# Kernel tuning notes

Measured on AMD Instinct MI355X. Metric: run time of the kernel, lower is better.

## Reference

```python
import jax, jax.numpy as jnp
import numpy as np

N, E = 20000, 640000
IN_CH, OUT_CH = 128, 64
HEADS = (4, 4)
NEG_SLOPE = 0.2


def _gat_layer(x, src, dst, edge_attr, edge_atten, W, a_src, a_dst, W_e, a_e, b, H, C, n_nodes):
    # x: [N, F_in] -> per-head features [N, H, C]
    xh = (x @ W).reshape(-1, H, C)
    alpha_src = jnp.sum(xh * a_src, axis=-1)          # [N, H]
    alpha_dst = jnp.sum(xh * a_dst, axis=-1)          # [N, H]
    eemb = (edge_attr @ W_e).reshape(-1, H, C)        # [E, H, C]
    alpha_e = jnp.sum(eemb * a_e, axis=-1)            # [E, H]
    alpha = alpha_src[src] + alpha_dst[dst] + alpha_e # [E, H]
    alpha = jax.nn.leaky_relu(alpha, NEG_SLOPE)
    # softmax over variable-degree neighborhoods (segments keyed by dst)
    amax = jax.ops.segment_max(alpha, dst, num_segments=n_nodes)
    alpha = jnp.exp(alpha - amax[dst])
    denom = jax.ops.segment_sum(alpha, dst, num_segments=n_nodes)
    alpha = alpha / (denom[dst] + 1e-16)
    msg = xh[src] * alpha[:, :, None]                 # [E, H, C]
    msg = msg * edge_atten[:, :, None]                # edge_atten: [E, 1] -> broadcast over H, C
    out = jax.ops.segment_sum(msg, dst, num_segments=n_nodes)
    out = out.reshape(n_nodes, H * C) + b
    return out, alpha


def setup_inputs() -> dict:
    key = jax.random.key(0)
    ks = jax.random.split(key, 16)
    H1, H2 = HEADS
    d1_in, d1_out = IN_CH, H1 * OUT_CH
    d2_in, d2_out = H1 * OUT_CH, H2 * OUT_CH
    s = lambda fi: 1.0 / np.sqrt(fi)
    inp = {
        "x": jax.random.normal(ks[0], (N, IN_CH), jnp.float32),
        "edge_index": jax.random.randint(ks[1], (2, E), 0, N, jnp.int64 if jax.config.jax_enable_x64 else jnp.int32),
        "batch": jnp.zeros((N,), jnp.int32),
        "edge_attr": jax.random.normal(ks[2], (E, 1), jnp.float32),
        "edge_atten": jax.random.uniform(ks[3], (E, 1), jnp.float32),
        # layer 1 params
        "W1": jax.random.normal(ks[4], (d1_in, d1_out), jnp.float32) * s(d1_in),
        "a_src1": jax.random.normal(ks[5], (H1, OUT_CH), jnp.float32) * s(OUT_CH),
        "a_dst1": jax.random.normal(ks[6], (H1, OUT_CH), jnp.float32) * s(OUT_CH),
        "W_e1": jax.random.normal(ks[7], (1, d1_out), jnp.float32),
        "a_e1": jax.random.normal(ks[8], (H1, OUT_CH), jnp.float32) * s(OUT_CH),
        "b1": jnp.zeros((d1_out,), jnp.float32),
        # layer 2 params
        "W2": jax.random.normal(ks[9], (d2_in, d2_out), jnp.float32) * s(d2_in),
        "a_src2": jax.random.normal(ks[10], (H2, OUT_CH), jnp.float32) * s(OUT_CH),
        "a_dst2": jax.random.normal(ks[11], (H2, OUT_CH), jnp.float32) * s(OUT_CH),
        "W_e2": jax.random.normal(ks[12], (1, d2_out), jnp.float32),
        "a_e2": jax.random.normal(ks[13], (H2, OUT_CH), jnp.float32) * s(OUT_CH),
        "b2": jnp.zeros((d2_out,), jnp.float32),
    }
    return inp


def reference(x, edge_index, batch, edge_attr, edge_atten,
              W1, a_src1, a_dst1, W_e1, a_e1, b1,
              W2, a_src2, a_dst2, W_e2, a_e2, b2):
    src, dst = edge_index[0], edge_index[1]
    h, w1 = _gat_layer(x, src, dst, edge_attr, edge_atten,
                       W1, a_src1, a_dst1, W_e1, a_e1, b1, HEADS[0], OUT_CH, N)
    h, w2 = _gat_layer(h, src, dst, edge_attr, edge_atten,
                       W2, a_src2, a_dst2, W_e2, a_e2, b2, HEADS[1], OUT_CH, N)
    return h, w1, w2
```

## Files before the change

### kernel.cpp

```cpp
#include <hip/hip_runtime.h>
#include <math.h>

#define NEG_SLOPE 0.2f
#define CAP 128
#define ST  136
#define NNODES 20000
#define NB 128

typedef short s16x8 __attribute__((ext_vector_type(8)));
typedef unsigned short us8 __attribute__((ext_vector_type(8)));
typedef float f32x4 __attribute__((ext_vector_type(4)));

__device__ __forceinline__ unsigned short f2bf(float f) {
    unsigned int u = __float_as_uint(f);
    return (unsigned short)((u + 0x7FFFu + ((u >> 16) & 1u)) >> 16);
}
__device__ __forceinline__ float bf2f(unsigned short s) {
    return __uint_as_float(((unsigned int)s) << 16);
}

__global__ __launch_bounds__(512) void hist_prep(const int* __restrict__ dst,
                                                 int* __restrict__ ghist,
                                                 int E, int chunk, int N, int histB,
                                                 const float* __restrict__ x,
                                                 const float* __restrict__ W1,
                                                 const float* __restrict__ W2,
                                                 const float* __restrict__ W_e1,
                                                 const float* __restrict__ a_e1,
                                                 const float* __restrict__ W_e2,
                                                 const float* __restrict__ a_e2,
                                                 unsigned short* __restrict__ xb16,
                                                 unsigned short* __restrict__ Wt1,
                                                 unsigned short* __restrict__ Wt2,
                                                 float* __restrict__ ce) {
    __shared__ int h[NNODES / 2];
    if ((int)blockIdx.x < histB) {
        const int b = blockIdx.x;
        const int NH = N >> 1;
        for (int i = threadIdx.x; i < NH; i += 512) h[i] = 0;
        __syncthreads();
        const int e0 = b * chunk;
        const int e1 = min(e0 + chunk, E);
        for (int e = e0 + (int)threadIdx.x; e < e1; e += 512) {
            int d = dst[e];
            atomicAdd(&h[d >> 1], 1 << ((d & 1) << 4));
        }
        __syncthreads();
        int2* out = (int2*)(ghist + (size_t)b * N);
        for (int i = threadIdx.x; i < NH; i += 512) {
            int v = h[i];
            out[i] = make_int2(v & 0xFFFF, ((unsigned)v) >> 16);
        }
    } else {
        const int p = (int)blockIdx.x - histB;
        const int gsz = 256 * 512;
        const int gid = p * 512 + (int)threadIdx.x;
        for (int i = gid; i < 128 * 256; i += gsz) {
            int k = i >> 8, n = i & 255;
            Wt1[n * 128 + k] = f2bf(W1[i]);
        }
        for (int i = gid; i < 256 * 256; i += gsz) {
            int k = i >> 8, n = i & 255;
            Wt2[n * 256 + k] = f2bf(W2[i]);
        }
        for (int i = gid; i < N * 32; i += gsz) {
            float4 f = ((const float4*)x)[i];
            ushort4 u = make_ushort4(f2bf(f.x), f2bf(f.y), f2bf(f.z), f2bf(f.w));
            ((ushort4*)xb16)[i] = u;
        }
        if (p < 2 && threadIdx.x < 256) {
            const float* We = p == 0 ? W_e1 : W_e2;
            const float* ae = p == 0 ? a_e1 : a_e2;
            int hh = threadIdx.x >> 6, c = threadIdx.x & 63;
            float pr = We[hh * 64 + c] * ae[hh * 64 + c];
#pragma unroll
            for (int off = 32; off > 0; off >>= 1) pr += __shfl_down(pr, off);
            if (c == 0) ce[p * 4 + hh] = pr;
        }
    }
}

__device__ __forceinline__ void gemm_core(const unsigned short* __restrict__ A16,
                                          const unsigned short* __restrict__ Bt16,
                                          unsigned short* __restrict__ C16,
                                          const float* __restrict__ a_src,
                                          const float* __restrict__ a_dst,
                                          float* __restrict__ asrc,
                                          float* __restrict__ adst,
                                          int M, int K, int bx, int by,
                                          unsigned short (*As)[40],
                                          unsigned short (*Bs)[40]) {
    const int tid = threadIdx.x;
    const int w = tid >> 6, l = tid & 63;
    const int quad = l >> 4, m16 = l & 15;
    const int row0 = by * 128, col0 = bx * 64;

    f32x4 acc[2][4] = {};

    const int a_r = tid >> 1;
    const int a_k = (tid & 1) * 16;
    const int b_n = tid >> 2;
    const int b_k = (tid & 3) * 8;

    for (int k0 = 0; k0 < K; k0 += 32) {
        int gr = row0 + a_r; if (gr > M - 1) gr = M - 1;
        const unsigned short* ap = A16 + (size_t)gr * K + k0 + a_k;
        *(us8*)&As[a_r][a_k]     = *(const us8*)ap;
        *(us8*)&As[a_r][a_k + 8] = *(const us8*)(ap + 8);
        *(us8*)&Bs[b_n][b_k] = *(const us8*)(Bt16 + (size_t)(col0 + b_n) * K + k0 + b_k);
        __syncthreads();

        s16x8 af[2], bfr[4];
#pragma unroll
        for (int mt = 0; mt < 2; ++mt)
            af[mt] = *(const s16x8*)&As[w * 32 + mt * 16 + m16][quad * 8];
#pragma unroll
        for (int nt = 0; nt < 4; ++nt)
            bfr[nt] = *(const s16x8*)&Bs[nt * 16 + m16][quad * 8];
#pragma unroll
        for (int mt = 0; mt < 2; ++mt)
#pragma unroll
            for (int nt = 0; nt < 4; ++nt)
                acc[mt][nt] = __builtin_amdgcn_mfma_f32_16x16x32_bf16(af[mt], bfr[nt], acc[mt][nt], 0, 0, 0);
        __syncthreads();
    }

    const int h = bx;
    float was[4], wad[4];
#pragma unroll
    for (int nt = 0; nt < 4; ++nt) {
        int c = nt * 16 + m16;
        was[nt] = a_src[h * 64 + c];
        wad[nt] = a_dst[h * 64 + c];
    }

#pragma unroll
    for (int mt = 0; mt < 2; ++mt)
#pragma unroll
        for (int i = 0; i < 4; ++i) {
            int row = row0 + w * 32 + mt * 16 + quad * 4 + i;
            float ps = 0.f, pd = 0.f;
#pragma unroll
            for (int nt = 0; nt < 4; ++nt) {
                float v = acc[mt][nt][i];
                ps += v * was[nt];
                pd += v * wad[nt];
            }
#pragma unroll
            for (int ofs = 1; ofs < 16; ofs <<= 1) {
                ps += __shfl_xor(ps, ofs);
                pd += __shfl_xor(pd, ofs);
            }
            if (m16 == 0 && row < M) {
                asrc[(size_t)row * 4 + h] = ps;
                adst[(size_t)row * 4 + h] = pd;
            }
        }

#pragma unroll
    for (int mt = 0; mt < 2; ++mt)
#pragma unroll
        for (int nt = 0; nt < 4; ++nt) {
            int col = col0 + nt * 16 + m16;
#pragma unroll
            for (int i = 0; i < 4; ++i) {
                int row = row0 + w * 32 + mt * 16 + quad * 4 + i;
                if (row < M) C16[(size_t)row * 256 + col] = f2bf(acc[mt][nt][i]);
            }
        }
}

__global__ __launch_bounds__(256) void gemm1_scan(const unsigned short* __restrict__ A16,
                                                  const unsigned short* __restrict__ Bt16,
                                                  unsigned short* __restrict__ C16,
                                                  const float* __restrict__ a_src,
                                                  const float* __restrict__ a_dst,
                                                  float* __restrict__ asrc,
                                                  float* __restrict__ adst,
                                                  int M, int K, int gemmB,
                                                  int* __restrict__ ghist,
                                                  int* __restrict__ deg,
                                                  int N, int histB) {
    __shared__ unsigned short As[128][40];
    __shared__ unsigned short Bs[64][40];
    if ((int)blockIdx.x < gemmB) {
        gemm_core(A16, Bt16, C16, a_src, a_dst, asrc, adst, M, K,
                  blockIdx.x & 3, blockIdx.x >> 2, As, Bs);
    } else {
        int bin = ((int)blockIdx.x - gemmB) * 256 + (int)threadIdx.x;
        if (bin < N) {
            int run = 0;
            for (int b = 0; b < histB; b += 8) {
                int v[8];
#pragma unroll
                for (int j = 0; j < 8; ++j) v[j] = ghist[(b + j) * N + bin];
#pragma unroll
                for (int j = 0; j < 8; ++j) { ghist[(b + j) * N + bin] = run; run += v[j]; }
            }
            deg[bin] = run;
        }
    }
}

__global__ __launch_bounds__(1024) void fill_scan(const int* __restrict__ src,
                                                  const int* __restrict__ dst,
                                                  const float* __restrict__ edge_attr,
                                                  const float* __restrict__ edge_atten,
                                                  const int* __restrict__ deg,
                                                  const int* __restrict__ ghist,
                                                  int* __restrict__ off_out,
                                                  int4* __restrict__ rec,
                                                  int E, int chunk, int N) {
    __shared__ int base[NNODES];
    __shared__ int wsum[16];
    __shared__ int woff[16];
    __shared__ int s_carry, s_bt;
    if (threadIdx.x == 0) s_carry = 0;
    __syncthreads();
    const int lane = threadIdx.x & 63, wid = threadIdx.x >> 6;
    for (int bb = 0; bb < N; bb += 4096) {
        int i0 = bb + (int)threadIdx.x * 4;
        int v0 = (i0 + 0 < N) ? deg[i0 + 0] : 0;
        int v1 = (i0 + 1 < N) ? deg[i0 + 1] : 0;
        int v2 = (i0 + 2 < N) ? deg[i0 + 2] : 0;
        int v3 = (i0 + 3 < N) ? deg[i0 + 3] : 0;
        int tsum = v0 + v1 + v2 + v3;
        int incl = tsum;
#pragma unroll
        for (int ofs = 1; ofs < 64; ofs <<= 1) {
            int t = __shfl_up(incl, ofs);
            if (lane >= ofs) incl += t;
        }
        if (lane == 63) wsum[wid] = incl;
        __syncthreads();
        if (wid == 0) {
            int ws = (lane < 16) ? wsum[lane] : 0;
            int wincl = ws;
#pragma unroll
            for (int ofs = 1; ofs < 16; ofs <<= 1) {
                int t = __shfl_up(wincl, ofs);
                if (lane >= ofs) wincl += t;
            }
            if (lane < 16) woff[lane] = wincl - ws;
            if (lane == 15) s_bt = wincl;
        }
        __syncthreads();
        int e0 = s_carry + woff[wid] + incl - tsum;
        int e1 = e0 + v0, e2 = e1 + v1, e3 = e2 + v2;
        if (i0 + 0 < N) base[i0 + 0] = e0;
        if (i0 + 1 < N) base[i0 + 1] = e1;
        if (i0 + 2 < N) base[i0 + 2] = e2;
        if (i0 + 3 < N) base[i0 + 3] = e3;
        __syncthreads();
        if (threadIdx.x == 0) s_carry += s_bt;
        __syncthreads();
    }
    if (blockIdx.x == 0) {
        for (int i = threadIdx.x; i < N; i += 1024) off_out[i] = base[i];
        if (threadIdx.x == 0) off_out[N] = s_carry;
    }
    const int b = blockIdx.x;
    const int* part = ghist + (size_t)b * N;
    for (int i = threadIdx.x; i < N; i += 1024) base[i] += part[i];
    __syncthreads();
    const int e0c = b * chunk;
    const int e1c = min(e0c + chunk, E);
    for (int e = e0c + (int)threadIdx.x; e < e1c; e += 1024) {
        int d = dst[e];
        int pos = atomicAdd(&base[d], 1);
        rec[pos] = make_int4(src[e], e, __float_as_int(edge_attr[e]),
                             __float_as_int(edge_atten[e]));
    }
}

__global__ __launch_bounds__(256) void node_fused(const int4* __restrict__ rec,
                                                  const int* __restrict__ off,
                                                  const float* __restrict__ asrc,
                                                  const float* __restrict__ adst,
                                                  const float* __restrict__ ce,
                                                  const unsigned short* __restrict__ xh16,
                                                  const float* __restrict__ bias,
                                                  float* __restrict__ w,
                                                  int write_w,
                                                  float* __restrict__ mxrc,
                                                  float* __restrict__ houtf,
                                                  unsigned short* __restrict__ hout16,
                                                  int N) {
    __shared__ float s_al[4][4][ST];
    __shared__ int s_src[4][CAP];
    const int wid = threadIdx.x >> 6;
    const int n = blockIdx.x * 4 + wid;
    if (n >= N) return;
    const int lane = threadIdx.x & 63;
    float* al = &s_al[wid][0][0];
    int* sv = s_src[wid];
    const int o0 = off[n], o1 = off[n + 1];
    const int deg = o1 - o0;

    const float4 c4 = *(const float4*)ce;
    const float4 ad4 = *(const float4*)(adst + (size_t)n * 4);

    if (deg <= 64) {
        int4 r; float4 a;
        a.x = a.y = a.z = a.w = -3.4e38f;
        if (lane < deg) {
            r = rec[o0 + lane];
            float ea = __int_as_float(r.z);
            const float4 as4 = *(const float4*)(asrc + (size_t)r.x * 4);
            a.x = as4.x + ad4.x + ea * c4.x;
            a.y = as4.y + ad4.y + ea * c4.y;
            a.z = as4.z + ad4.z + ea * c4.z;
            a.w = as4.w + ad4.w + ea * c4.w;
            a.x = a.x > 0.f ? a.x : NEG_SLOPE * a.x;
            a.y = a.y > 0.f ? a.y : NEG_SLOPE * a.y;
            a.z = a.z > 0.f ? a.z : NEG_SLOPE * a.z;
            a.w = a.w > 0.f ? a.w : NEG_SLOPE * a.w;
        }
        float4 mx = a;
#pragma unroll
        for (int ofs = 1; ofs < 64; ofs <<= 1) {
            mx.x = fmaxf(mx.x, __shfl_xor(mx.x, ofs));
            mx.y = fmaxf(mx.y, __shfl_xor(mx.y, ofs));
            mx.z = fmaxf(mx.z, __shfl_xor(mx.z, ofs));
            mx.w = fmaxf(mx.w, __shfl_xor(mx.w, ofs));
        }
        float4 ex = make_float4(0.f, 0.f, 0.f, 0.f);
        if (lane < deg) {
            ex.x = __expf(a.x - mx.x);
            ex.y = __expf(a.y - mx.y);
            ex.z = __expf(a.z - mx.z);
            ex.w = __expf(a.w - mx.w);
        }
        float4 sm = ex;
#pragma unroll
        for (int ofs = 1; ofs < 64; ofs <<= 1) {
            sm.x += __shfl_xor(sm.x, ofs);
            sm.y += __shfl_xor(sm.y, ofs);
            sm.z += __shfl_xor(sm.z, ofs);
            sm.w += __shfl_xor(sm.w, ofs);
        }
        float4 rc;
        rc.x = 1.f / (sm.x + 1e-16f);
        rc.y = 1.f / (sm.y + 1e-16f);
        rc.z = 1.f / (sm.z + 1e-16f);
        rc.w = 1.f / (sm.w + 1e-16f);
        if (mxrc && lane == 0) {
            *(float4*)(mxrc + (size_t)n * 8) = mx;
            *(float4*)(mxrc + (size_t)n * 8 + 4) = rc;
        }
        if (lane < deg) {
            float4 aln;
            aln.x = ex.x * rc.x;
            aln.y = ex.y * rc.y;
            aln.z = ex.z * rc.z;
            aln.w = ex.w * rc.w;
            if (write_w) *(float4*)(w + (size_t)r.y * 4) = aln;
            float att = __int_as_float(r.w);
            sv[lane] = r.x;
            al[0 * ST + lane] = aln.x * att;
            al[1 * ST + lane] = aln.y * att;
            al[2 * ST + lane] = aln.z * att;
            al[3 * ST + lane] = aln.w * att;
        }
    } else {
        float4 mx = make_float4(-3.4e38f, -3.4e38f, -3.4e38f, -3.4e38f);
        for (int idx = lane; idx < deg; idx += 64) {
            int4 r = rec[o0 + idx];
            float ea = __int_as_float(r.z);
            const float4 as4 = *(const float4*)(asrc + (size_t)r.x * 4);
            float4 a;
            a.x = as4.x + ad4.x + ea * c4.x;
            a.y = as4.y + ad4.y + ea * c4.y;
            a.z = as4.z + ad4.z + ea * c4.z;
            a.w = as4.w + ad4.w + ea * c4.w;
            a.x = a.x > 0.f ? a.x : NEG_SLOPE * a.x;
            a.y = a.y > 0.f ? a.y : NEG_SLOPE * a.y;
            a.z = a.z > 0.f ? a.z : NEG_SLOPE * a.z;
            a.w = a.w > 0.f ? a.w : NEG_SLOPE * a.w;
            if (idx < CAP) {
                sv[idx] = r.x;
                al[0 * ST + idx] = a.x;
                al[1 * ST + idx] = a.y;
                al[2 * ST + idx] = a.z;
                al[3 * ST + idx] = a.w;
            } else {
                *(float4*)(w + (size_t)r.y * 4) = a;
            }
            mx.x = fmaxf(mx.x, a.x);
            mx.y = fmaxf(mx.y, a.y);
            mx.z = fmaxf(mx.z, a.z);
            mx.w = fmaxf(mx.w, a.w);
        }
#pragma unroll
        for (int ofs = 1; ofs < 64; ofs <<= 1) {
            mx.x = fmaxf(mx.x, __shfl_xor(mx.x, ofs));
            mx.y = fmaxf(mx.y, __shfl_xor(mx.y, ofs));
            mx.z = fmaxf(mx.z, __shfl_xor(mx.z, ofs));
            mx.w = fmaxf(mx.w, __shfl_xor(mx.w, ofs));
        }
        float4 sm = make_float4(0.f, 0.f, 0.f, 0.f);
        for (int idx = lane; idx < deg; idx += 64) {
            float4 a;
            int espill = -1;
            if (idx < CAP) {
                a.x = al[0 * ST + idx];
                a.y = al[1 * ST + idx];
                a.z = al[2 * ST + idx];
                a.w = al[3 * ST + idx];
            } else {
                espill = rec[o0 + idx].y;
                a = *(const float4*)(w + (size_t)espill * 4);
            }
            a.x = __expf(a.x - mx.x);
            a.y = __expf(a.y - mx.y);
            a.z = __expf(a.z - mx.z);
            a.w = __expf(a.w - mx.w);
            if (idx < CAP) {
                al[0 * ST + idx] = a.x;
                al[1 * ST + idx] = a.y;
                al[2 * ST + idx] = a.z;
                al[3 * ST + idx] = a.w;
            } else {
                *(float4*)(w + (size_t)espill * 4) = a;
            }
            sm.x += a.x; sm.y += a.y; sm.z += a.z; sm.w += a.w;
        }
#pragma unroll
        for (int ofs = 1; ofs < 64; ofs <<= 1) {
            sm.x += __shfl_xor(sm.x, ofs);
            sm.y += __shfl_xor(sm.y, ofs);
            sm.z += __shfl_xor(sm.z, ofs);
            sm.w += __shfl_xor(sm.w, ofs);
        }
        float4 rc;
        rc.x = 1.f / (sm.x + 1e-16f);
        rc.y = 1.f / (sm.y + 1e-16f);
        rc.z = 1.f / (sm.z + 1e-16f);
        rc.w = 1.f / (sm.w + 1e-16f);
        if (mxrc && lane == 0) {
            *(float4*)(mxrc + (size_t)n * 8) = mx;
            *(float4*)(mxrc + (size_t)n * 8 + 4) = rc;
        }
        for (int idx = lane; idx < deg; idx += 64) {
            int4 r = rec[o0 + idx];
            float4 ex;
            if (idx < CAP) {
                ex.x = al[0 * ST + idx];
                ex.y = al[1 * ST + idx];
                ex.z = al[2 * ST + idx];
                ex.w = al[3 * ST + idx];
            } else {
                ex = *(const float4*)(w + (size_t)r.y * 4);
            }
            float4 aln;
            aln.x = ex.x * rc.x;
            aln.y = ex.y * rc.y;
            aln.z = ex.z * rc.z;
            aln.w = ex.w * rc.w;
            *(float4*)(w + (size_t)r.y * 4) = aln;
            if (idx < CAP) {
                float att = __int_as_float(r.w);
                al[0 * ST + idx] = aln.x * att;
                al[1 * ST + idx] = aln.y * att;
                al[2 * ST + idx] = aln.z * att;
                al[3 * ST + idx] = aln.w * att;
            }
        }
    }

    const int hh = lane >> 4;
    const float* alh = al + hh * ST;
    float4 a0 = *(const float4*)(bias + lane * 4);
    float4 a1 = make_float4(0.f, 0.f, 0.f, 0.f);
    float4 a2 = a1, a3 = a1;
    const int kmax = deg < CAP ? deg : CAP;
    int k = 0;
    for (; k + 8 <= kmax; k += 8) {
        int4 s4a = *(const int4*)&sv[k];
        int4 s4b = *(const int4*)&sv[k + 4];
        float4 ca = *(const float4*)&alh[k];
        float4 cb = *(const float4*)&alh[k + 4];
        ushort4 u0 = *((const ushort4*)(xh16 + (size_t)s4a.x * 256) + lane);
        ushort4 u1 = *((const ushort4*)(xh16 + (size_t)s4a.y * 256) + lane);
        ushort4 u2 = *((const ushort4*)(xh16 + (size_t)s4a.z * 256) + lane);
        ushort4 u3 = *((const ushort4*)(xh16 + (size_t)s4a.w * 256) + lane);
        ushort4 u4 = *((const ushort4*)(xh16 + (size_t)s4b.x * 256) + lane);
        ushort4 u5 = *((const ushort4*)(xh16 + (size_t)s4b.y * 256) + lane);
        ushort4 u6 = *((const ushort4*)(xh16 + (size_t)s4b.z * 256) + lane);
        ushort4 u7 = *((const ushort4*)(xh16 + (size_t)s4b.w * 256) + lane);
        a0.x += bf2f(u0.x) * ca.x; a0.y += bf2f(u0.y) * ca.x; a0.z += bf2f(u0.z) * ca.x; a0.w += bf2f(u0.w) * ca.x;
        a1.x += bf2f(u1.x) * ca.y; a1.y += bf2f(u1.y) * ca.y; a1.z += bf2f(u1.z) * ca.y; a1.w += bf2f(u1.w) * ca.y;
        a2.x += bf2f(u2.x) * ca.z; a2.y += bf2f(u2.y) * ca.z; a2.z += bf2f(u2.z) * ca.z; a2.w += bf2f(u2.w) * ca.z;
        a3.x += bf2f(u3.x) * ca.w; a3.y += bf2f(u3.y) * ca.w; a3.z += bf2f(u3.z) * ca.w; a3.w += bf2f(u3.w) * ca.w;
        a0.x += bf2f(u4.x) * cb.x; a0.y += bf2f(u4.y) * cb.x; a0.z += bf2f(u4.z) * cb.x; a0.w += bf2f(u4.w) * cb.x;
        a1.x += bf2f(u5.x) * cb.y; a1.y += bf2f(u5.y) * cb.y; a1.z += bf2f(u5.z) * cb.y; a1.w += bf2f(u5.w) * cb.y;
        a2.x += bf2f(u6.x) * cb.z; a2.y += bf2f(u6.y) * cb.z; a2.z += bf2f(u6.z) * cb.z; a2.w += bf2f(u6.w) * cb.z;
        a3.x += bf2f(u7.x) * cb.w; a3.y += bf2f(u7.y) * cb.w; a3.z += bf2f(u7.z) * cb.w; a3.w += bf2f(u7.w) * cb.w;
    }
    for (; k + 4 <= kmax; k += 4) {
        int4 s4 = *(const int4*)&sv[k];
        float4 cc = *(const float4*)&alh[k];
        ushort4 u0 = *((const ushort4*)(xh16 + (size_t)s4.x * 256) + lane);
        ushort4 u1 = *((const ushort4*)(xh16 + (size_t)s4.y * 256) + lane);
        ushort4 u2 = *((const ushort4*)(xh16 + (size_t)s4.z * 256) + lane);
        ushort4 u3 = *((const ushort4*)(xh16 + (size_t)s4.w * 256) + lane);
        a0.x += bf2f(u0.x) * cc.x; a0.y += bf2f(u0.y) * cc.x; a0.z += bf2f(u0.z) * cc.x; a0.w += bf2f(u0.w) * cc.x;
        a1.x += bf2f(u1.x) * cc.y; a1.y += bf2f(u1.y) * cc.y; a1.z += bf2f(u1.z) * cc.y; a1.w += bf2f(u1.w) * cc.y;
        a2.x += bf2f(u2.x) * cc.z; a2.y += bf2f(u2.y) * cc.z; a2.z += bf2f(u2.z) * cc.z; a2.w += bf2f(u2.w) * cc.z;
        a3.x += bf2f(u3.x) * cc.w; a3.y += bf2f(u3.y) * cc.w; a3.z += bf2f(u3.z) * cc.w; a3.w += bf2f(u3.w) * cc.w;
    }
    for (; k < kmax; ++k) {
        int s = sv[k];
        float sc = alh[k];
        ushort4 uv = *((const ushort4*)(xh16 + (size_t)s * 256) + lane);
        a0.x += bf2f(uv.x) * sc; a0.y += bf2f(uv.y) * sc;
        a0.z += bf2f(uv.z) * sc; a0.w += bf2f(uv.w) * sc;
    }
    for (k = CAP; k < deg; ++k) {
        int4 r = rec[o0 + k];
        float sc = w[(size_t)r.y * 4 + hh] * __int_as_float(r.w);
        ushort4 uv = *((const ushort4*)(xh16 + (size_t)r.x * 256) + lane);
        a0.x += bf2f(uv.x) * sc; a0.y += bf2f(uv.y) * sc;
        a0.z += bf2f(uv.z) * sc; a0.w += bf2f(uv.w) * sc;
    }
    float4 acc;
    acc.x = (a0.x + a1.x) + (a2.x + a3.x);
    acc.y = (a0.y + a1.y) + (a2.y + a3.y);
    acc.z = (a0.z + a1.z) + (a2.z + a3.z);
    acc.w = (a0.w + a1.w) + (a2.w + a3.w);
    if (houtf)  *(float4*)(houtf + (size_t)n * 256 + lane * 4) = acc;
    if (hout16) {
        ushort4 u = make_ushort4(f2bf(acc.x), f2bf(acc.y), f2bf(acc.z), f2bf(acc.w));
        *((ushort4*)(hout16 + (size_t)n * 256) + lane) = u;
    }
}

__global__ __launch_bounds__(256) void gemm2_w1(const unsigned short* __restrict__ A16,
                                                const unsigned short* __restrict__ Bt16,
                                                unsigned short* __restrict__ C16,
                                                const float* __restrict__ a_src,
                                                const float* __restrict__ a_dst,
                                                float* __restrict__ asrc2,
                                                float* __restrict__ adst2,
                                                int M, int K, int gemmB,
                                                const int* __restrict__ src,
                                                const int* __restrict__ dstp,
                                                const float* __restrict__ edge_attr,
                                                const float* __restrict__ asrc1,
                                                const float* __restrict__ adst1,
                                                const float* __restrict__ mxrc,
                                                const float* __restrict__ ce1,
                                                float* __restrict__ w1, int E) {
    __shared__ unsigned short As[128][40];
    __shared__ unsigned short Bs[64][40];
    if ((int)blockIdx.x < gemmB) {
        gemm_core(A16, Bt16, C16, a_src, a_dst, asrc2, adst2, M, K,
                  blockIdx.x & 3, blockIdx.x >> 2, As, Bs);
    } else {
        const int stride = ((int)gridDim.x - gemmB) * 256;
        const float4 c4 = *(const float4*)ce1;
        for (int e = ((int)blockIdx.x - gemmB) * 256 + (int)threadIdx.x; e < E; e += stride) {
            int s = src[e], d = dstp[e];
            float ea = edge_attr[e];
            const float4 as4 = *(const float4*)(asrc1 + (size_t)s * 4);
            const float4 ad4 = *(const float4*)(adst1 + (size_t)d * 4);
            float4 a;
            a.x = as4.x + ad4.x + ea * c4.x;
            a.y = as4.y + ad4.y + ea * c4.y;
            a.z = as4.z + ad4.z + ea * c4.z;
            a.w = as4.w + ad4.w + ea * c4.w;
            a.x = a.x > 0.f ? a.x : NEG_SLOPE * a.x;
            a.y = a.y > 0.f ? a.y : NEG_SLOPE * a.y;
            a.z = a.z > 0.f ? a.z : NEG_SLOPE * a.z;
            a.w = a.w > 0.f ? a.w : NEG_SLOPE * a.w;
            const float4 mx = *(const float4*)(mxrc + (size_t)d * 8);
            const float4 rc = *(const float4*)(mxrc + (size_t)d * 8 + 4);
            float4 o;
            o.x = __expf(a.x - mx.x) * rc.x;
            o.y = __expf(a.y - mx.y) * rc.y;
            o.z = __expf(a.z - mx.z) * rc.z;
            o.w = __expf(a.w - mx.w) * rc.w;
            *(float4*)(w1 + (size_t)e * 4) = o;
        }
    }
}

extern "C" void kernel_launch(void* const* d_in, const int* in_sizes, int n_in,
                              void* d_out, int out_size, void* d_ws, size_t ws_size,
                              hipStream_t stream) {
    const float* x          = (const float*)d_in[0];
    const int*   ei         = (const int*)d_in[1];
    const float* edge_attr  = (const float*)d_in[3];
    const float* edge_atten = (const float*)d_in[4];
    const float* W1     = (const float*)d_in[5];
    const float* a_src1 = (const float*)d_in[6];
    const float* a_dst1 = (const float*)d_in[7];
    const float* W_e1   = (const float*)d_in[8];
    const float* a_e1   = (const float*)d_in[9];
    const float* b1     = (const float*)d_in[10];
    const float* W2     = (const float*)d_in[11];
    const float* a_src2 = (const float*)d_in[12];
    const float* a_dst2 = (const float*)d_in[13];
    const float* W_e2   = (const float*)d_in[14];
    const float* a_e2   = (const float*)d_in[15];
    const float* b2     = (const float*)d_in[16];

    const int N = in_sizes[0] / 128;
    const int E = in_sizes[1] / 2;
    const int* srcp = ei;
    const int* dstp = ei + E;

    char* ws = (char*)d_ws;
    int4* rec             = (int4*)ws;            ws += (size_t)E * 16;
    unsigned short* xh16  = (unsigned short*)ws;  ws += (size_t)N * 256 * 2;
    unsigned short* h116  = (unsigned short*)ws;  ws += (size_t)N * 256 * 2;
    unsigned short* Wt1   = (unsigned short*)ws;  ws += (size_t)256 * 128 * 2;
    unsigned short* Wt2   = (unsigned short*)ws;  ws += (size_t)256 * 256 * 2;
    float* asrc   = (float*)ws;                   ws += (size_t)N * 4 * 4;
    float* adst   = (float*)ws;                   ws += (size_t)N * 4 * 4;
    float* asrc2  = (float*)ws;                   ws += (size_t)N * 4 * 4;
    float* adst2  = (float*)ws;                   ws += (size_t)N * 4 * 4;
    float* mxrc   = (float*)ws;                   ws += (size_t)N * 8 * 4;
    float* ce     = (float*)ws;                   ws += 32;
    int* deg    = (int*)ws;                       ws += (size_t)N * 4;
    int* off    = (int*)ws;                       ws += (size_t)(N + 1) * 4;
    int* ghist  = (int*)ws;                       ws += (size_t)NB * N * 4;

    unsigned short* xb16 = h116;

    float* hout2 = (float*)d_out;
    float* w1    = hout2 + (size_t)N * 256;
    float* w2    = w1 + (size_t)E * 4;

    const int chunk = (E + NB - 1) / NB;
    const int gb = (N + 3) / 4;
    const int rows = (N + 127) / 128;
    const int gemmB = 4 * rows;
    const int scanB = (N + 255) / 256;
    const int wB = 512;

    hist_prep<<<NB + 256, 512, 0, stream>>>(dstp, ghist, E, chunk, N, NB,
                                            x, W1, W2, W_e1, a_e1, W_e2, a_e2,
                                            xb16, Wt1, Wt2, ce);
    gemm1_scan<<<gemmB + scanB, 256, 0, stream>>>(xb16, Wt1, xh16, a_src1, a_dst1,
                                                  asrc, adst, N, 128, gemmB,
                                                  ghist, deg, N, NB);
    fill_scan<<<NB, 1024, 0, stream>>>(srcp, dstp, edge_attr, edge_atten,
                                       deg, ghist, off, rec, E, chunk, N);
    node_fused<<<gb, 256, 0, stream>>>(rec, off, asrc, adst, ce, xh16, b1, w1,
                                       0, mxrc, (float*)nullptr, h116, N);
    gemm2_w1<<<gemmB + wB, 256, 0, stream>>>(h116, Wt2, xh16, a_src2, a_dst2,
                                             asrc2, adst2, N, 256, gemmB,
                                             srcp, dstp, edge_attr,
                                             asrc, adst, mxrc, ce, w1, E);
    node_fused<<<gb, 256, 0, stream>>>(rec, off, asrc2, adst2, ce + 4, xh16, b2, w2,
                                       1, (float*)nullptr, hout2,
                                       (unsigned short*)nullptr, N);
}
```

Baseline: 253.6 us.

## Widen GEMM tiles to 128x128 with K-step 64 and halve histogram blocks

The shared GEMM core now computes a 128x128 output tile per block, covering two heads, with a K step of 64. Each block therefore does more MFMA work per shared-memory load and per barrier, and the grid has half as many GEMM blocks. The per-head attention projections are split inside each tile. Separately, the number of histogram chunks drops from 128 to 64, which shrinks the per-bin scan and the ghist buffer but leaves fewer blocks for the histogram and fill stages. The cost is more registers (16 accumulators) and more LDS per block, which may lower occupancy.

After: 263.3 us. +3.8%, slower.

```diff
diff --git a/kernel.cpp b/kernel.cpp
--- a/kernel.cpp
+++ b/kernel.cpp
@@ -5,7 +5,7 @@
 #define CAP 128
 #define ST  136
 #define NNODES 20000
-#define NB 128
+#define NB 64
 
 typedef short s16x8 __attribute__((ext_vector_type(8)));
 typedef unsigned short us8 __attribute__((ext_vector_type(8)));
@@ -88,48 +88,56 @@
                                           float* __restrict__ asrc,
                                           float* __restrict__ adst,
                                           int M, int K, int bx, int by,
-                                          unsigned short (*As)[40],
-                                          unsigned short (*Bs)[40]) {
+                                          unsigned short (*As)[72],
+                                          unsigned short (*Bs)[72]) {
     const int tid = threadIdx.x;
     const int w = tid >> 6, l = tid & 63;
     const int quad = l >> 4, m16 = l & 15;
-    const int row0 = by * 128, col0 = bx * 64;
-
-    f32x4 acc[2][4] = {};
+    const int row0 = by * 128, col0 = bx * 128;
+
+    f32x4 acc[2][8] = {};
 
     const int a_r = tid >> 1;
-    const int a_k = (tid & 1) * 16;
-    const int b_n = tid >> 2;
-    const int b_k = (tid & 3) * 8;
-
-    for (int k0 = 0; k0 < K; k0 += 32) {
+    const int a_k = (tid & 1) * 32;
+
+    for (int k0 = 0; k0 < K; k0 += 64) {
         int gr = row0 + a_r; if (gr > M - 1) gr = M - 1;
         const unsigned short* ap = A16 + (size_t)gr * K + k0 + a_k;
-        *(us8*)&As[a_r][a_k]     = *(const us8*)ap;
-        *(us8*)&As[a_r][a_k + 8] = *(const us8*)(ap + 8);
-        *(us8*)&Bs[b_n][b_k] = *(const us8*)(Bt16 + (size_t)(col0 + b_n) * K + k0 + b_k);
-        __syncthreads();
-
-        s16x8 af[2], bfr[4];
-#pragma unroll
-        for (int mt = 0; mt < 2; ++mt)
-            af[mt] = *(const s16x8*)&As[w * 32 + mt * 16 + m16][quad * 8];
-#pragma unroll
-        for (int nt = 0; nt < 4; ++nt)
-            bfr[nt] = *(const s16x8*)&Bs[nt * 16 + m16][quad * 8];
-#pragma unroll
-        for (int mt = 0; mt < 2; ++mt)
-#pragma unroll
-            for (int nt = 0; nt < 4; ++nt)
-                acc[mt][nt] = __builtin_amdgcn_mfma_f32_16x16x32_bf16(af[mt], bfr[nt], acc[mt][nt], 0, 0, 0);
-        __syncthreads();
-    }
-
-    const int h = bx;
-    float was[4], wad[4];
-#pragma unroll
-    for (int nt = 0; nt < 4; ++nt) {
-        int c = nt * 16 + m16;
+        *(us8*)&As[a_r][a_k]      = *(const us8*)ap;
+        *(us8*)&As[a_r][a_k + 8]  = *(const us8*)(ap + 8);
+        *(us8*)&As[a_r][a_k + 16] = *(const us8*)(ap + 16);
+        *(us8*)&As[a_r][a_k + 24] = *(const us8*)(ap + 24);
+        const unsigned short* bp = Bt16 + (size_t)(col0 + a_r) * K + k0 + a_k;
+        *(us8*)&Bs[a_r][a_k]      = *(const us8*)bp;
+        *(us8*)&Bs[a_r][a_k + 8]  = *(const us8*)(bp + 8);
+        *(us8*)&Bs[a_r][a_k + 16] = *(const us8*)(bp + 16);
+        *(us8*)&Bs[a_r][a_k + 24] = *(const us8*)(bp + 24);
+        __syncthreads();
+
+#pragma unroll
+        for (int sub = 0; sub < 2; ++sub) {
+            s16x8 af[2], bfr[8];
+#pragma unroll
+            for (int mt = 0; mt < 2; ++mt)
+                af[mt] = *(const s16x8*)&As[w * 32 + mt * 16 + m16][sub * 32 + quad * 8];
+#pragma unroll
+            for (int nt = 0; nt < 8; ++nt)
+                bfr[nt] = *(const s16x8*)&Bs[nt * 16 + m16][sub * 32 + quad * 8];
+#pragma unroll
+            for (int mt = 0; mt < 2; ++mt)
+#pragma unroll
+                for (int nt = 0; nt < 8; ++nt)
+                    acc[mt][nt] = __builtin_amdgcn_mfma_f32_16x16x32_bf16(af[mt], bfr[nt], acc[mt][nt], 0, 0, 0);
+        }
+        __syncthreads();
+    }
+
+    const int h0 = col0 >> 6;
+    float was[8], wad[8];
+#pragma unroll
+    for (int nt = 0; nt < 8; ++nt) {
+        int h = h0 + (nt >> 2);
+        int c = (nt & 3) * 16 + m16;
         was[nt] = a_src[h * 64 + c];
         wad[nt] = a_dst[h * 64 + c];
     }
@@ -139,28 +147,31 @@
 #pragma unroll
         for (int i = 0; i < 4; ++i) {
             int row = row0 + w * 32 + mt * 16 + quad * 4 + i;
-            float ps = 0.f, pd = 0.f;
-#pragma unroll
-            for (int nt = 0; nt < 4; ++nt) {
-                float v = acc[mt][nt][i];
-                ps += v * was[nt];
-                pd += v * wad[nt];
-            }
-#pragma unroll
-            for (int ofs = 1; ofs < 16; ofs <<= 1) {
-                ps += __shfl_xor(ps, ofs);
-                pd += __shfl_xor(pd, ofs);
-            }
-            if (m16 == 0 && row < M) {
-                asrc[(size_t)row * 4 + h] = ps;
-                adst[(size_t)row * 4 + h] = pd;
+#pragma unroll
+            for (int p = 0; p < 2; ++p) {
+                float ps = 0.f, pd = 0.f;
+#pragma unroll
+                for (int nt = p * 4; nt < p * 4 + 4; ++nt) {
+                    float v = acc[mt][nt][i];
+                    ps += v * was[nt];
+                    pd += v * wad[nt];
+                }
+#pragma unroll
+                for (int ofs = 1; ofs < 16; ofs <<= 1) {
+                    ps += __shfl_xor(ps, ofs);
+                    pd += __shfl_xor(pd, ofs);
+                }
+                if (m16 == 0 && row < M) {
+                    asrc[(size_t)row * 4 + h0 + p] = ps;
+                    adst[(size_t)row * 4 + h0 + p] = pd;
+                }
             }
         }
 
 #pragma unroll
     for (int mt = 0; mt < 2; ++mt)
 #pragma unroll
-        for (int nt = 0; nt < 4; ++nt) {
+        for (int nt = 0; nt < 8; ++nt) {
             int col = col0 + nt * 16 + m16;
 #pragma unroll
             for (int i = 0; i < 4; ++i) {
@@ -181,11 +192,11 @@
                                                   int* __restrict__ ghist,
                                                   int* __restrict__ deg,
                                                   int N, int histB) {
-    __shared__ unsigned short As[128][40];
-    __shared__ unsigned short Bs[64][40];
+    __shared__ unsigned short As[128][72];
+    __shared__ unsigned short Bs[128][72];
     if ((int)blockIdx.x < gemmB) {
         gemm_core(A16, Bt16, C16, a_src, a_dst, asrc, adst, M, K,
-                  blockIdx.x & 3, blockIdx.x >> 2, As, Bs);
+                  blockIdx.x & 1, blockIdx.x >> 1, As, Bs);
     } else {
         int bin = ((int)blockIdx.x - gemmB) * 256 + (int)threadIdx.x;
         if (bin < N) {
@@ -551,11 +562,11 @@
                                                 const float* __restrict__ mxrc,
                                                 const float* __restrict__ ce1,
                                                 float* __restrict__ w1, int E) {
-    __shared__ unsigned short As[128][40];
-    __shared__ unsigned short Bs[64][40];
+    __shared__ unsigned short As[128][72];
+    __shared__ unsigned short Bs[128][72];
     if ((int)blockIdx.x < gemmB) {
         gemm_core(A16, Bt16, C16, a_src, a_dst, asrc2, adst2, M, K,
-                  blockIdx.x & 3, blockIdx.x >> 2, As, Bs);
+                  blockIdx.x & 1, blockIdx.x >> 1, As, Bs);
     } else {
         const int stride = ((int)gridDim.x - gemmB) * 256;
         const float4 c4 = *(const float4*)ce1;
@@ -635,7 +646,7 @@
     const int chunk = (E + NB - 1) / NB;
     const int gb = (N + 3) / 4;
     const int rows = (N + 127) / 128;
-    const int gemmB = 4 * rows;
+    const int gemmB = 2 * rows;
     const int scanB = (N + 255) / 256;
     const int wB = 512;
 
```

## Fuse fp32-to-bf16 conversion into layer-1 GEMM and co-schedule it with histogram

Applied to the files above, without the earlier changes.

Layer 1's GEMM now reads x and W1 directly in fp32 and converts them to bf16 while filling shared memory. This removes the separate conversion pass that wrote x and a transposed W1 out as bf16. That GEMM now runs in the same launch as the dst histogram and the W2 prep. The column scan moves into its own small kernel, so the launch count stays the same. In exchange the GEMM loads twice as many bytes, and its B tile is read with strided scalar loads.

Result: slower. 265.6 us (+4.7%).

```diff
diff --git a/kernel.cpp b/kernel.cpp
--- a/kernel.cpp
+++ b/kernel.cpp
@@ -19,69 +19,10 @@
     return __uint_as_float(((unsigned int)s) << 16);
 }
 
-__global__ __launch_bounds__(512) void hist_prep(const int* __restrict__ dst,
-                                                 int* __restrict__ ghist,
-                                                 int E, int chunk, int N, int histB,
-                                                 const float* __restrict__ x,
-                                                 const float* __restrict__ W1,
-                                                 const float* __restrict__ W2,
-                                                 const float* __restrict__ W_e1,
-                                                 const float* __restrict__ a_e1,
-                                                 const float* __restrict__ W_e2,
-                                                 const float* __restrict__ a_e2,
-                                                 unsigned short* __restrict__ xb16,
-                                                 unsigned short* __restrict__ Wt1,
-                                                 unsigned short* __restrict__ Wt2,
-                                                 float* __restrict__ ce) {
-    __shared__ int h[NNODES / 2];
-    if ((int)blockIdx.x < histB) {
-        const int b = blockIdx.x;
-        const int NH = N >> 1;
-        for (int i = threadIdx.x; i < NH; i += 512) h[i] = 0;
-        __syncthreads();
-        const int e0 = b * chunk;
-        const int e1 = min(e0 + chunk, E);
-        for (int e = e0 + (int)threadIdx.x; e < e1; e += 512) {
-            int d = dst[e];
-            atomicAdd(&h[d >> 1], 1 << ((d & 1) << 4));
-        }
-        __syncthreads();
-        int2* out = (int2*)(ghist + (size_t)b * N);
-        for (int i = threadIdx.x; i < NH; i += 512) {
-            int v = h[i];
-            out[i] = make_int2(v & 0xFFFF, ((unsigned)v) >> 16);
-        }
-    } else {
-        const int p = (int)blockIdx.x - histB;
-        const int gsz = 256 * 512;
-        const int gid = p * 512 + (int)threadIdx.x;
-        for (int i = gid; i < 128 * 256; i += gsz) {
-            int k = i >> 8, n = i & 255;
-            Wt1[n * 128 + k] = f2bf(W1[i]);
-        }
-        for (int i = gid; i < 256 * 256; i += gsz) {
-            int k = i >> 8, n = i & 255;
-            Wt2[n * 256 + k] = f2bf(W2[i]);
-        }
-        for (int i = gid; i < N * 32; i += gsz) {
-            float4 f = ((const float4*)x)[i];
-            ushort4 u = make_ushort4(f2bf(f.x), f2bf(f.y), f2bf(f.z), f2bf(f.w));
-            ((ushort4*)xb16)[i] = u;
-        }
-        if (p < 2 && threadIdx.x < 256) {
-            const float* We = p == 0 ? W_e1 : W_e2;
-            const float* ae = p == 0 ? a_e1 : a_e2;
-            int hh = threadIdx.x >> 6, c = threadIdx.x & 63;
-            float pr = We[hh * 64 + c] * ae[hh * 64 + c];
-#pragma unroll
-            for (int off = 32; off > 0; off >>= 1) pr += __shfl_down(pr, off);
-            if (c == 0) ce[p * 4 + hh] = pr;
-        }
-    }
-}
-
 __device__ __forceinline__ void gemm_core(const unsigned short* __restrict__ A16,
+                                          const float* __restrict__ A32,
                                           const unsigned short* __restrict__ Bt16,
+                                          const float* __restrict__ B32,
                                           unsigned short* __restrict__ C16,
                                           const float* __restrict__ a_src,
                                           const float* __restrict__ a_dst,
@@ -104,10 +45,31 @@
 
     for (int k0 = 0; k0 < K; k0 += 32) {
         int gr = row0 + a_r; if (gr > M - 1) gr = M - 1;
-        const unsigned short* ap = A16 + (size_t)gr * K + k0 + a_k;
-        *(us8*)&As[a_r][a_k]     = *(const us8*)ap;
-        *(us8*)&As[a_r][a_k + 8] = *(const us8*)(ap + 8);
-        *(us8*)&Bs[b_n][b_k] = *(const us8*)(Bt16 + (size_t)(col0 + b_n) * K + k0 + b_k);
+        if (A32) {
+            const float* ap = A32 + (size_t)gr * K + k0 + a_k;
+            float4 f0 = *(const float4*)(ap);
+            float4 f1 = *(const float4*)(ap + 4);
+            float4 f2 = *(const float4*)(ap + 8);
+            float4 f3 = *(const float4*)(ap + 12);
+            unsigned short* d0 = &As[a_r][a_k];
+            d0[0] = f2bf(f0.x); d0[1] = f2bf(f0.y); d0[2] = f2bf(f0.z); d0[3] = f2bf(f0.w);
+            d0[4] = f2bf(f1.x); d0[5] = f2bf(f1.y); d0[6] = f2bf(f1.z); d0[7] = f2bf(f1.w);
+            d0[8] = f2bf(f2.x); d0[9] = f2bf(f2.y); d0[10] = f2bf(f2.z); d0[11] = f2bf(f2.w);
+            d0[12] = f2bf(f3.x); d0[13] = f2bf(f3.y); d0[14] = f2bf(f3.z); d0[15] = f2bf(f3.w);
+        } else {
+            const unsigned short* ap = A16 + (size_t)gr * K + k0 + a_k;
+            *(us8*)&As[a_r][a_k]     = *(const us8*)ap;
+            *(us8*)&As[a_r][a_k + 8] = *(const us8*)(ap + 8);
+        }
+        if (B32) {
+            const float* bp = B32 + (size_t)(k0 + b_k) * 256 + col0 + b_n;
+            unsigned short t[8];
+#pragma unroll
+            for (int j = 0; j < 8; ++j) t[j] = f2bf(bp[(size_t)j * 256]);
+            *(us8*)&Bs[b_n][b_k] = *(const us8*)t;
+        } else {
+            *(us8*)&Bs[b_n][b_k] = *(const us8*)(Bt16 + (size_t)(col0 + b_n) * K + k0 + b_k);
+        }
         __syncthreads();
 
         s16x8 af[2], bfr[4];
@@ -170,35 +132,83 @@
         }
 }
 
-__global__ __launch_bounds__(256) void gemm1_scan(const unsigned short* __restrict__ A16,
-                                                  const unsigned short* __restrict__ Bt16,
-                                                  unsigned short* __restrict__ C16,
-                                                  const float* __restrict__ a_src,
-                                                  const float* __restrict__ a_dst,
-                                                  float* __restrict__ asrc,
-                                                  float* __restrict__ adst,
-                                                  int M, int K, int gemmB,
-                                                  int* __restrict__ ghist,
-                                                  int* __restrict__ deg,
-                                                  int N, int histB) {
-    __shared__ unsigned short As[128][40];
-    __shared__ unsigned short Bs[64][40];
-    if ((int)blockIdx.x < gemmB) {
-        gemm_core(A16, Bt16, C16, a_src, a_dst, asrc, adst, M, K,
-                  blockIdx.x & 3, blockIdx.x >> 2, As, Bs);
+__global__ __launch_bounds__(256) void hist_gemm1_prep(const int* __restrict__ dst,
+                                                       int* __restrict__ ghist,
+                                                       int E, int chunk, int N,
+                                                       int histB, int gemmB,
+                                                       const float* __restrict__ x,
+                                                       const float* __restrict__ W1,
+                                                       const float* __restrict__ W2,
+                                                       const float* __restrict__ W_e1,
+                                                       const float* __restrict__ a_e1,
+                                                       const float* __restrict__ W_e2,
+                                                       const float* __restrict__ a_e2,
+                                                       unsigned short* __restrict__ Wt2,
+                                                       float* __restrict__ ce,
+                                                       unsigned short* __restrict__ xh16,
+                                                       const float* __restrict__ a_src1,
+                                                       const float* __restrict__ a_dst1,
+                                                       float* __restrict__ asrc,
+                                                       float* __restrict__ adst,
+                                                       int M) {
+    __shared__ int smem[NNODES / 2];
+    if ((int)blockIdx.x < histB) {
+        const int b = blockIdx.x;
+        const int NH = N >> 1;
+        for (int i = threadIdx.x; i < NH; i += 256) smem[i] = 0;
+        __syncthreads();
+        const int e0 = b * chunk;
+        const int e1 = min(e0 + chunk, E);
+        for (int e = e0 + (int)threadIdx.x; e < e1; e += 256) {
+            int d = dst[e];
+            atomicAdd(&smem[d >> 1], 1 << ((d & 1) << 4));
+        }
+        __syncthreads();
+        int2* out = (int2*)(ghist + (size_t)b * N);
+        for (int i = threadIdx.x; i < NH; i += 256) {
+            int v = smem[i];
+            out[i] = make_int2(v & 0xFFFF, ((unsigned)v) >> 16);
+        }
+    } else if ((int)blockIdx.x < histB + gemmB) {
+        int g = (int)blockIdx.x - histB;
+        gemm_core((const unsigned short*)nullptr, x, (const unsigned short*)nullptr, W1,
+                  xh16, a_src1, a_dst1, asrc, adst, M, 128, g & 3, g >> 2,
+                  (unsigned short(*)[40])smem,
+                  (unsigned short(*)[40])((char*)smem + 10240));
     } else {
-        int bin = ((int)blockIdx.x - gemmB) * 256 + (int)threadIdx.x;
-        if (bin < N) {
-            int run = 0;
-            for (int b = 0; b < histB; b += 8) {
-                int v[8];
-#pragma unroll
-                for (int j = 0; j < 8; ++j) v[j] = ghist[(b + j) * N + bin];
-#pragma unroll
-                for (int j = 0; j < 8; ++j) { ghist[(b + j) * N + bin] = run; run += v[j]; }
-            }
-            deg[bin] = run;
-        }
+        const int p = (int)blockIdx.x - histB - gemmB;
+        const int gsz = 32 * 256;
+        const int gid = p * 256 + (int)threadIdx.x;
+        for (int i = gid; i < 256 * 256; i += gsz) {
+            int k = i >> 8, n = i & 255;
+            Wt2[n * 256 + k] = f2bf(W2[i]);
+        }
+        if (p < 2) {
+            const float* We = p == 0 ? W_e1 : W_e2;
+            const float* ae = p == 0 ? a_e1 : a_e2;
+            int hh = threadIdx.x >> 6, c = threadIdx.x & 63;
+            float pr = We[hh * 64 + c] * ae[hh * 64 + c];
+#pragma unroll
+            for (int off = 32; off > 0; off >>= 1) pr += __shfl_down(pr, off);
+            if (c == 0) ce[p * 4 + hh] = pr;
+        }
+    }
+}
+
+__global__ __launch_bounds__(256) void colscan(int* __restrict__ ghist,
+                                               int* __restrict__ deg,
+                                               int N, int histB) {
+    int bin = blockIdx.x * 256 + (int)threadIdx.x;
+    if (bin < N) {
+        int run = 0;
+        for (int b = 0; b < histB; b += 8) {
+            int v[8];
+#pragma unroll
+            for (int j = 0; j < 8; ++j) v[j] = ghist[(b + j) * N + bin];
+#pragma unroll
+            for (int j = 0; j < 8; ++j) { ghist[(b + j) * N + bin] = run; run += v[j]; }
+        }
+        deg[bin] = run;
     }
 }
 
@@ -554,7 +564,8 @@
     __shared__ unsigned short As[128][40];
     __shared__ unsigned short Bs[64][40];
     if ((int)blockIdx.x < gemmB) {
-        gemm_core(A16, Bt16, C16, a_src, a_dst, asrc2, adst2, M, K,
+        gemm_core(A16, (const float*)nullptr, Bt16, (const float*)nullptr,
+                  C16, a_src, a_dst, asrc2, adst2, M, K,
                   blockIdx.x & 3, blockIdx.x >> 2, As, Bs);
     } else {
         const int stride = ((int)gridDim.x - gemmB) * 256;
@@ -614,7 +625,6 @@
     int4* rec             = (int4*)ws;            ws += (size_t)E * 16;
     unsigned short* xh16  = (unsigned short*)ws;  ws += (size_t)N * 256 * 2;
     unsigned short* h116  = (unsigned short*)ws;  ws += (size_t)N * 256 * 2;
-    unsigned short* Wt1   = (unsigned short*)ws;  ws += (size_t)256 * 128 * 2;
     unsigned short* Wt2   = (unsigned short*)ws;  ws += (size_t)256 * 256 * 2;
     float* asrc   = (float*)ws;                   ws += (size_t)N * 4 * 4;
     float* adst   = (float*)ws;                   ws += (size_t)N * 4 * 4;
@@ -626,8 +636,6 @@
     int* off    = (int*)ws;                       ws += (size_t)(N + 1) * 4;
     int* ghist  = (int*)ws;                       ws += (size_t)NB * N * 4;
 
-    unsigned short* xb16 = h116;
-
     float* hout2 = (float*)d_out;
     float* w1    = hout2 + (size_t)N * 256;
     float* w2    = w1 + (size_t)E * 4;
@@ -639,12 +647,13 @@
     const int scanB = (N + 255) / 256;
     const int wB = 512;
 
-    hist_prep<<<NB + 256, 512, 0, stream>>>(dstp, ghist, E, chunk, N, NB,
-                                            x, W1, W2, W_e1, a_e1, W_e2, a_e2,
-                                            xb16, Wt1, Wt2, ce);
-    gemm1_scan<<<gemmB + scanB, 256, 0, stream>>>(xb16, Wt1, xh16, a_src1, a_dst1,
-                                                  asrc, adst, N, 128, gemmB,
-                                                  ghist, deg, N, NB);
+    hist_gemm1_prep<<<NB + gemmB + 32, 256, 0, stream>>>(dstp, ghist, E, chunk, N,
+                                                         NB, gemmB,
+                                                         x, W1, W2, W_e1, a_e1,
+                                                         W_e2, a_e2, Wt2, ce,
+                                                         xh16, a_src1, a_dst1,
+                                                         asrc, adst, N);
+    colscan<<<scanB, 256, 0, stream>>>(ghist, deg, N, NB);
     fill_scan<<<NB, 1024, 0, stream>>>(srcp, dstp, edge_attr, edge_atten,
                                        deg, ghist, off, rec, E, chunk, N);
     node_fused<<<gb, 256, 0, stream>>>(rec, off, asrc, adst, ce, xh16, b1, w1,
```
